# Kernel tuning notes

Measured on AMD Instinct MI355X. Metric: run time of the kernel, lower is better.

The kernel has to match this reference:

```python
import jax, jax.numpy as jnp
import numpy as np
import math

D = 768      # embedding_dim
H = 12       # attn_n_heads
HD = D // H  # head_dim = 64
F = 3072     # ff_latent_dim
B, S = 1, 4096
EPS = 1e-5


def setup_inputs() -> dict:
    key = jax.random.key(0)
    ks = jax.random.split(key, 16)
    s = 0.02
    return {
        "x": jax.random.normal(ks[0], (B, S, D), jnp.float32),
        # per-head Q/K/V projections stacked: [H, D, HD]
        "Wq": jax.random.normal(ks[1], (H, D, HD), jnp.float32) * s,
        "bq": jnp.zeros((H, HD), jnp.float32),
        "Wk": jax.random.normal(ks[2], (H, D, HD), jnp.float32) * s,
        "bk": jnp.zeros((H, HD), jnp.float32),
        "Wv": jax.random.normal(ks[3], (H, D, HD), jnp.float32) * s,
        "bv": jnp.zeros((H, HD), jnp.float32),
        "Wo": jax.random.normal(ks[4], (D, D), jnp.float32) * s,
        "bo": jnp.zeros((D,), jnp.float32),
        "ln1_w": jnp.ones((D,), jnp.float32),
        "ln1_b": jnp.zeros((D,), jnp.float32),
        "ln2_w": jnp.ones((D,), jnp.float32),
        "ln2_b": jnp.zeros((D,), jnp.float32),
        "W1": jax.random.normal(ks[5], (D, F), jnp.float32) * s,
        "b1": jnp.zeros((F,), jnp.float32),
        "W2": jax.random.normal(ks[6], (F, D), jnp.float32) * s,
        "b2": jnp.zeros((D,), jnp.float32),
    }


def _layer_norm(z, w, b):
    mu = jnp.mean(z, axis=-1, keepdims=True)
    var = jnp.mean(jnp.square(z - mu), axis=-1, keepdims=True)
    return (z - mu) * jax.lax.rsqrt(var + EPS) * w + b


def reference(x, Wq, bq, Wk, bk, Wv, bv, Wo, bo,
              ln1_w, ln1_b, ln2_w, ln2_b, W1, b1, W2, b2):
    # pre-norm attention block
    y = _layer_norm(x, ln1_w, ln1_b)
    q = jnp.einsum('bsd,hde->bhse', y, Wq) + bq[None, :, None, :]
    k = jnp.einsum('bsd,hde->bhse', y, Wk) + bk[None, :, None, :]
    v = jnp.einsum('bsd,hde->bhse', y, Wv) + bv[None, :, None, :]
    scores = jnp.einsum('bhqe,bhke->bhqk', q, k) * (1.0 / math.sqrt(HD))
    attn = jax.nn.softmax(scores, axis=-1)            # [B,H,S,S]
    o = jnp.einsum('bhqk,bhke->bhqe', attn, v)        # [B,H,S,HD]
    o = o.transpose(0, 2, 1, 3).reshape(x.shape[0], x.shape[1], D)  # concat heads
    o = o @ Wo + bo
    x = x + o
    # pre-norm FFN block (eval mode: dropout is identity)
    y = _layer_norm(x, ln2_w, ln2_b)
    h = jax.nn.gelu(y @ W1 + b1, approximate=False)   # torch F.gelu default = exact erf
    x = x + (h @ W2 + b2)
    return x
```

## Files before the change

### kernel.cpp

```cpp
#include <hip/hip_runtime.h>
#include <stdint.h>

typedef __bf16 bf16;
typedef __bf16 bf16x2 __attribute__((ext_vector_type(2)));
typedef __bf16 bf16x4 __attribute__((ext_vector_type(4)));
typedef __bf16 bf16x8 __attribute__((ext_vector_type(8)));
typedef float f32x4 __attribute__((ext_vector_type(4)));
typedef float f32x16 __attribute__((ext_vector_type(16)));
typedef uint32_t u32;
typedef unsigned int u32x2 __attribute__((ext_vector_type(2)));

#define QSCALE 0.1803368801111137f

__device__ __forceinline__ float fast_exp2(float x) {
#if __has_builtin(__builtin_amdgcn_exp2f)
  return __builtin_amdgcn_exp2f(x);
#else
  return exp2f(x);
#endif
}

__device__ __forceinline__ u32 pack_bf16(float a, float b) {
  bf16x2 v; v[0] = (bf16)a; v[1] = (bf16)b;
  return __builtin_bit_cast(u32, v);
}

__device__ __forceinline__ void permswap32(u32& a, u32& b) {
#if __has_builtin(__builtin_amdgcn_permlane32_swap)
  u32x2 r = __builtin_amdgcn_permlane32_swap(a, b, false, false);
  a = r[0]; b = r[1];
#else
  asm volatile("v_permlane32_swap_b32 %0, %1" : "+v"(a), "+v"(b));
#endif
}

__device__ __forceinline__ void async16(void* lds, const void* g) {
  __builtin_amdgcn_global_load_lds(
      (__attribute__((address_space(1))) uint32_t*)(uintptr_t)g,
      (__attribute__((address_space(3))) uint32_t*)(uint32_t)(uintptr_t)lds,
      16, 0, 0);
}

__global__ __launch_bounds__(256) void conv_qkv_w_kernel(
    const float* __restrict__ Wq, const float* __restrict__ Wk,
    const float* __restrict__ Wv, bf16* __restrict__ out)
{
  __shared__ float tile[32][33];
  int z = blockIdx.z;
  int part = z / 12, h = z - part * 12;
  const float* W = (part == 0) ? Wq : (part == 1) ? Wk : Wv;
  float sc = (part == 0) ? QSCALE : 1.0f;
  int bd = blockIdx.x * 32, be = blockIdx.y * 32;
  int tc = threadIdx.x & 31, tr = threadIdx.x >> 5;
  #pragma unroll
  for (int i = 0; i < 4; i++)
    tile[tr + i * 8][tc] = W[((size_t)h * 768 + bd + tr + i * 8) * 64 + be + tc] * sc;
  __syncthreads();
  #pragma unroll
  for (int i = 0; i < 4; i++) {
    int e = be + tr + i * 8;
    out[(size_t)(part * 768 + h * 64 + e) * 768 + bd + tc] = (bf16)tile[tc][tr + i * 8];
  }
}

__global__ __launch_bounds__(256) void conv_qkv_b_kernel(
    const float* __restrict__ bq, const float* __restrict__ bk,
    const float* __restrict__ bv, float* __restrict__ out)
{
  int n = blockIdx.x * 256 + threadIdx.x;
  int part = n / 768, nn = n - part * 768;
  const float* B = (part == 0) ? bq : (part == 1) ? bk : bv;
  float v = B[nn];
  if (part == 0) v *= QSCALE;
  out[n] = v;
}

__global__ __launch_bounds__(256) void transpose_tile_kernel(
    const float* __restrict__ in, bf16* __restrict__ out, int R, int C)
{
  __shared__ float tile[32][33];
  int bc = blockIdx.x * 32, br = blockIdx.y * 32;
  int tc = threadIdx.x & 31, tr = threadIdx.x >> 5;
  #pragma unroll
  for (int i = 0; i < 4; i++)
    tile[tr + i * 8][tc] = in[(size_t)(br + tr + i * 8) * C + bc + tc];
  __syncthreads();
  #pragma unroll
  for (int i = 0; i < 4; i++) {
    int c = bc + tr + i * 8;
    out[(size_t)c * R + br + tc] = (bf16)tile[tc][tr + i * 8];
  }
}

__global__ __launch_bounds__(256) void reduce_add_kernel(
    float* __restrict__ out, const bf16* __restrict__ p)
{
  int i = blockIdx.x * 256 + threadIdx.x;
  float4 o = ((float4*)out)[i];
  bf16x4 v = ((const bf16x4*)p)[i];
  o.x += (float)v[0]; o.y += (float)v[1];
  o.z += (float)v[2]; o.w += (float)v[3];
  ((float4*)out)[i] = o;
}

__global__ __launch_bounds__(256) void ln_kernel(
    const float* __restrict__ x, const float* __restrict__ w,
    const float* __restrict__ b, bf16* __restrict__ y)
{
  int row = blockIdx.x;
  const float* xr = x + (size_t)row * 768;
  int t = threadIdx.x;
  float v0 = xr[t], v1 = xr[t + 256], v2 = xr[t + 512];
  float s = v0 + v1 + v2, s2 = v0 * v0 + v1 * v1 + v2 * v2;
  #pragma unroll
  for (int d = 1; d < 64; d <<= 1) {
    s  += __shfl_xor(s, d, 64);
    s2 += __shfl_xor(s2, d, 64);
  }
  __shared__ float red[8];
  int wv = t >> 6, ln = t & 63;
  if (ln == 0) { red[wv] = s; red[4 + wv] = s2; }
  __syncthreads();
  s  = red[0] + red[1] + red[2] + red[3];
  s2 = red[4] + red[5] + red[6] + red[7];
  float mu = s * (1.0f / 768.0f);
  float var = s2 * (1.0f / 768.0f) - mu * mu;
  float rstd = rsqrtf(var + 1e-5f);
  bf16* yr = y + (size_t)row * 768;
  yr[t]       = (bf16)((v0 - mu) * rstd * w[t]       + b[t]);
  yr[t + 256] = (bf16)((v1 - mu) * rstd * w[t + 256] + b[t + 256]);
  yr[t + 512] = (bf16)((v2 - mu) * rstd * w[t + 512] + b[t + 512]);
}

__global__ __launch_bounds__(256) void ln_add_kernel(
    float* __restrict__ x1, const bf16* __restrict__ p,
    const float* __restrict__ w, const float* __restrict__ b,
    bf16* __restrict__ y)
{
  int row = blockIdx.x;
  float* xr = x1 + (size_t)row * 768;
  const bf16* pr = p + (size_t)row * 768;
  int t = threadIdx.x;
  float v0 = xr[t]       + (float)pr[t];
  float v1 = xr[t + 256] + (float)pr[t + 256];
  float v2 = xr[t + 512] + (float)pr[t + 512];
  xr[t] = v0; xr[t + 256] = v1; xr[t + 512] = v2;
  float s = v0 + v1 + v2, s2 = v0 * v0 + v1 * v1 + v2 * v2;
  #pragma unroll
  for (int d = 1; d < 64; d <<= 1) {
    s  += __shfl_xor(s, d, 64);
    s2 += __shfl_xor(s2, d, 64);
  }
  __shared__ float red[8];
  int wv = t >> 6, ln = t & 63;
  if (ln == 0) { red[wv] = s; red[4 + wv] = s2; }
  __syncthreads();
  s  = red[0] + red[1] + red[2] + red[3];
  s2 = red[4] + red[5] + red[6] + red[7];
  float mu = s * (1.0f / 768.0f);
  float var = s2 * (1.0f / 768.0f) - mu * mu;
  float rstd = rsqrtf(var + 1e-5f);
  bf16* yr = y + (size_t)row * 768;
  yr[t]       = (bf16)((v0 - mu) * rstd * w[t]       + b[t]);
  yr[t + 256] = (bf16)((v1 - mu) * rstd * w[t + 256] + b[t + 256]);
  yr[t + 512] = (bf16)((v2 - mu) * rstd * w[t + 512] + b[t + 512]);
}

template <int MODE>
__global__ __launch_bounds__(256) void gemm_bt(
    const bf16* __restrict__ A, const bf16* __restrict__ Bt,
    const float* __restrict__ bias, const float* __restrict__ res,
    void* __restrict__ outp, void* __restrict__ out2, int M, int N, int K)
{
  __shared__ bf16 As[128 * 32];
  __shared__ bf16 Bs[128 * 32];
  int t = threadIdx.x;
  int w = t >> 6, lane = t & 63;
  int quad = lane >> 4, l16 = lane & 15;
  int tile_m = blockIdx.y * 128, tile_n = blockIdx.x * 128;

  int srow = lane >> 2;
  int skb = (lane & 3) * 8;
  const bf16* Ag = A  + (size_t)(tile_m + w * 16 + srow) * K + skb;
  const bf16* Bg = Bt + (size_t)(tile_n + w * 16 + srow) * K + skb;
  char* AsB = (char*)As + w * 1024;
  char* BsB = (char*)Bs + w * 1024;
  size_t rstep = (size_t)64 * K;

  int wm = (w >> 1) * 64, wn = (w & 1) * 64;
  f32x4 acc[4][4] = {};

  int kbeg = 0, kend = K;
  if (MODE == 5) {
    int half = K >> 1;
    kbeg = blockIdx.z * half;
    kend = kbeg + half;
  }

  for (int k0 = kbeg; k0 < kend; k0 += 32) {
    __syncthreads();
    async16(AsB,        Ag + k0);
    async16(AsB + 4096, Ag + rstep + k0);
    async16(BsB,        Bg + k0);
    async16(BsB + 4096, Bg + rstep + k0);
    __syncthreads();

    bf16x8 af[4], bfr[4];
    #pragma unroll
    for (int mb = 0; mb < 4; mb++)
      af[mb] = *(const bf16x8*)(As + (wm + mb * 16 + l16) * 32 + quad * 8);
    #pragma unroll
    for (int nb = 0; nb < 4; nb++)
      bfr[nb] = *(const bf16x8*)(Bs + (wn + nb * 16 + l16) * 32 + quad * 8);
    #pragma unroll
    for (int mb = 0; mb < 4; mb++)
      #pragma unroll
      for (int nb = 0; nb < 4; nb++)
        acc[mb][nb] = __builtin_amdgcn_mfma_f32_16x16x32_bf16(
            af[mb], bfr[nb], acc[mb][nb], 0, 0, 0);
  }

  #pragma unroll
  for (int mb = 0; mb < 4; mb++) {
    #pragma unroll
    for (int nb = 0; nb < 4; nb++) {
      int col = tile_n + wn + nb * 16 + l16;
      int row0 = tile_m + wm + mb * 16 + quad * 4;
      if (MODE == 4) {
        float bc = bias[col];
        if (col < 1536) {
          #pragma unroll
          for (int r = 0; r < 4; r++)
            ((bf16*)outp)[(size_t)(row0 + r) * 1536 + col] =
                (bf16)(acc[mb][nb][r] + bc);
        } else {
          bf16x4 pk;
          #pragma unroll
          for (int r = 0; r < 4; r++) pk[r] = (bf16)(acc[mb][nb][r] + bc);
          *(bf16x4*)((bf16*)out2 + (size_t)(col - 1536) * 4096 + row0) = pk;
        }
      } else if (MODE == 2) {
        float bc = bias[col];
        #pragma unroll
        for (int r = 0; r < 4; r++) {
          size_t idx = (size_t)(row0 + r) * N + col;
          float v = acc[mb][nb][r] + bc;
          float g = 0.5f * v * (1.0f + erff(v * 0.70710678118654752f));
          ((bf16*)outp)[idx] = (bf16)g;
        }
      } else {
        if (blockIdx.z == 0) {
          float bc = bias[col];
          #pragma unroll
          for (int r = 0; r < 4; r++) {
            size_t idx = (size_t)(row0 + r) * N + col;
            ((float*)outp)[idx] = res[idx] + acc[mb][nb][r] + bc;
          }
        } else {
          #pragma unroll
          for (int r = 0; r < 4; r++) {
            size_t idx = (size_t)(row0 + r) * N + col;
            ((bf16*)out2)[idx] = (bf16)acc[mb][nb][r];
          }
        }
      }
    }
  }
}

__global__ __launch_bounds__(256) void flash_kernel(
    const bf16* __restrict__ qk, const bf16* __restrict__ vtg,
    bf16* __restrict__ Opart, float* __restrict__ Lpart)
{
  __shared__ char smem[49152];
  bf16* Qs = (bf16*)smem;
  int t = threadIdx.x, w = t >> 6, lane = t & 63;
  int l32 = lane & 31, hi = lane >> 5;
  int qt = blockIdx.x, h = blockIdx.y, z = blockIdx.z;
  int q0 = qt * 128, kv0 = z * 2048;
  int qsel = w & 1, ksel = w >> 1;
  int qw = qsel * 64, kb = ksel * 32;

  int srow = lane >> 3, scol = ((lane & 7) ^ srow) * 8;

  #pragma unroll
  for (int c = 0; c < 4; c++) {
    const bf16* qg = qk + (size_t)(q0 + c * 32 + w * 8 + srow) * 1536 + h * 64 + scol;
    async16(smem + c * 4096 + w * 1024, qg);
  }

  const bf16* kg = qk + 768 + h * 64 + (size_t)(kv0 + w * 8 + srow) * 1536 + scol;
  const bf16* vg = vtg + (size_t)(h * 64 + w * 8 + srow) * 4096 + kv0 + scol;

  {
    char* kb0 = smem + 16384 + w * 1024;
    char* vb0 = smem + 32768 + w * 1024;
    async16(kb0,        kg);
    async16(kb0 + 4096, kg + (size_t)32 * 1536);
    async16(vb0,        vg);
    async16(vb0 + 4096, vg + (size_t)32 * 4096);
  }
  __syncthreads();

  int qr0 = qw + l32, qr1 = qw + 32 + l32;
  bf16x8 qf0[4], qf1[4];
  #pragma unroll
  for (int ks = 0; ks < 4; ks++) {
    qf0[ks] = *(const bf16x8*)(Qs + qr0 * 64 + (((ks * 2 + hi) ^ (qr0 & 7)) * 8));
    qf1[ks] = *(const bf16x8*)(Qs + qr1 * 64 + (((ks * 2 + hi) ^ (qr1 & 7)) * 8));
  }

  f32x16 oT00 = {}, oT10 = {}, oT01 = {}, oT11 = {};
  float l0 = 0.0f, l1 = 0.0f;
  int krow = kb + l32;
  int er0 = l32, er1 = 32 + l32;

  for (int j = 0; j < 32; j++) {
    int cur = j & 1;
    if (j < 31) {
      const bf16* kgn = kg + (size_t)(j + 1) * 64 * 1536;
      const bf16* vgn = vg + (j + 1) * 64;
      char* kbn = smem + 16384 + (cur ^ 1) * 8192 + w * 1024;
      char* vbn = smem + 32768 + (cur ^ 1) * 8192 + w * 1024;
      async16(kbn,        kgn);
      async16(kbn + 4096, kgn + (size_t)32 * 1536);
      async16(vbn,        vgn);
      async16(vbn + 4096, vgn + (size_t)32 * 4096);
    }
    const bf16* Ks = (const bf16*)(smem + 16384 + cur * 8192);
    const bf16* Vs = (const bf16*)(smem + 32768 + cur * 8192);

    f32x16 s0 = {}, s1 = {};
    __builtin_amdgcn_s_setprio(1);
    #pragma unroll
    for (int ks = 0; ks < 4; ks++) {
      bf16x8 kf = *(const bf16x8*)(Ks + krow * 64 + (((ks * 2 + hi) ^ (krow & 7)) * 8));
      s0 = __builtin_amdgcn_mfma_f32_32x32x16_bf16(kf, qf0[ks], s0, 0, 0, 0);
      s1 = __builtin_amdgcn_mfma_f32_32x32x16_bf16(kf, qf1[ks], s1, 0, 0, 0);
    }
    __builtin_amdgcn_s_setprio(0);

    bf16x8 pf00, pf01, pf10, pf11;
    {
      float p[16];
      #pragma unroll
      for (int i = 0; i < 16; i++) p[i] = fast_exp2(s0[i]);
      float t0 = (p[0] + p[1]) + (p[2] + p[3]);
      float t1 = (p[4] + p[5]) + (p[6] + p[7]);
      float t2 = (p[8] + p[9]) + (p[10] + p[11]);
      float t3 = (p[12] + p[13]) + (p[14] + p[15]);
      l0 += (t0 + t1) + (t2 + t3);
      u32 dd[8];
      #pragma unroll
      for (int k = 0; k < 8; k++) dd[k] = pack_bf16(p[2 * k], p[2 * k + 1]);
      permswap32(dd[0], dd[2]);
      permswap32(dd[1], dd[3]);
      permswap32(dd[4], dd[6]);
      permswap32(dd[5], dd[7]);
      pf00 = __builtin_bit_cast(bf16x8, uint4{dd[0], dd[1], dd[2], dd[3]});
      pf01 = __builtin_bit_cast(bf16x8, uint4{dd[4], dd[5], dd[6], dd[7]});
    }
    {
      float p[16];
      #pragma unroll
      for (int i = 0; i < 16; i++) p[i] = fast_exp2(s1[i]);
      float t0 = (p[0] + p[1]) + (p[2] + p[3]);
      float t1 = (p[4] + p[5]) + (p[6] + p[7]);
      float t2 = (p[8] + p[9]) + (p[10] + p[11]);
      float t3 = (p[12] + p[13]) + (p[14] + p[15]);
      l1 += (t0 + t1) + (t2 + t3);
      u32 dd[8];
      #pragma unroll
      for (int k = 0; k < 8; k++) dd[k] = pack_bf16(p[2 * k], p[2 * k + 1]);
      permswap32(dd[0], dd[2]);
      permswap32(dd[1], dd[3]);
      permswap32(dd[4], dd[6]);
      permswap32(dd[5], dd[7]);
      pf10 = __builtin_bit_cast(bf16x8, uint4{dd[0], dd[1], dd[2], dd[3]});
      pf11 = __builtin_bit_cast(bf16x8, uint4{dd[4], dd[5], dd[6], dd[7]});
    }

    __builtin_amdgcn_s_setprio(1);
    #pragma unroll
    for (int kstep = 0; kstep < 2; kstep++) {
      int grp = (kb >> 3) + kstep * 2 + hi;
      bf16x8 va = *(const bf16x8*)(Vs + er0 * 64 + ((grp ^ (er0 & 7)) * 8));
      bf16x8 vb = *(const bf16x8*)(Vs + er1 * 64 + ((grp ^ (er1 & 7)) * 8));
      bf16x8 pa = kstep ? pf01 : pf00;
      bf16x8 pb = kstep ? pf11 : pf10;
      oT00 = __builtin_amdgcn_mfma_f32_32x32x16_bf16(va, pa, oT00, 0, 0, 0);
      oT10 = __builtin_amdgcn_mfma_f32_32x32x16_bf16(vb, pa, oT10, 0, 0, 0);
      oT01 = __builtin_amdgcn_mfma_f32_32x32x16_bf16(va, pb, oT01, 0, 0, 0);
      oT11 = __builtin_amdgcn_mfma_f32_32x32x16_bf16(vb, pb, oT11, 0, 0, 0);
    }
    __builtin_amdgcn_s_setprio(0);

    __syncthreads();
  }

  float lq0 = l0 + __shfl_xor(l0, 32, 64);
  float lq1 = l1 + __shfl_xor(l1, 32, 64);
  float* OS = (float*)smem;
  float* LS = (float*)(smem + 34304);
  if (ksel == 1) {
    #pragma unroll
    for (int i = 0; i < 16; i++) {
      int eoff = (i & 3) + 8 * (i >> 2) + 4 * hi;
      OS[qr0 * 67 + eoff]      = oT00[i];
      OS[qr0 * 67 + 32 + eoff] = oT10[i];
      OS[qr1 * 67 + eoff]      = oT01[i];
      OS[qr1 * 67 + 32 + eoff] = oT11[i];
    }
    if (hi == 0) { LS[qr0] = lq0; LS[qr1] = lq1; }
  }
  __syncthreads();
  if (ksel == 0) {
    size_t tb = ((size_t)z * 12 + h) * 32 + qt;
    float la0 = lq0 + LS[qr0], la1 = lq1 + LS[qr1];
    if (hi == 0) { Lpart[tb * 128 + qr0] = la0; Lpart[tb * 128 + qr1] = la1; }
    bf16* ob0 = Opart + tb * 8192 + (size_t)qr0 * 64;
    bf16* ob1 = Opart + tb * 8192 + (size_t)qr1 * 64;
    #pragma unroll
    for (int g = 0; g < 4; g++) {
      int e0 = 8 * g + 4 * hi;
      bf16x4 a0, a1, b0, b1;
      #pragma unroll
      for (int r = 0; r < 4; r++) {
        a0[r] = (bf16)(oT00[g * 4 + r] + OS[qr0 * 67 + e0 + r]);
        a1[r] = (bf16)(oT10[g * 4 + r] + OS[qr0 * 67 + 32 + e0 + r]);
        b0[r] = (bf16)(oT01[g * 4 + r] + OS[qr1 * 67 + e0 + r]);
        b1[r] = (bf16)(oT11[g * 4 + r] + OS[qr1 * 67 + 32 + e0 + r]);
      }
      *(bf16x4*)(ob0 + e0)      = a0;
      *(bf16x4*)(ob0 + 32 + e0) = a1;
      *(bf16x4*)(ob1 + e0)      = b0;
      *(bf16x4*)(ob1 + 32 + e0) = b1;
    }
  }
}

__global__ __launch_bounds__(256) void flash_combine_kernel(
    const bf16* __restrict__ Opart, const float* __restrict__ Lpart,
    bf16* __restrict__ o)
{
  int qt = blockIdx.x, h = blockIdx.y;
  int t = threadIdx.x;
  size_t t0 = (size_t)h * 32 + qt;
  size_t t1 = (size_t)(12 + h) * 32 + qt;
  #pragma unroll
  for (int qq = 0; qq < 2; qq++) {
    int q = qq * 64 + (t >> 2), eg = (t & 3) * 16;
    float inv = 1.0f / (Lpart[t0 * 128 + q] + Lpart[t1 * 128 + q]);
    const bf16* p0 = Opart + t0 * 8192 + (size_t)q * 64 + eg;
    const bf16* p1 = Opart + t1 * 8192 + (size_t)q * 64 + eg;
    bf16x8 a0 = *(const bf16x8*)p0, a1 = *(const bf16x8*)(p0 + 8);
    bf16x8 b0 = *(const bf16x8*)p1, b1 = *(const bf16x8*)(p1 + 8);
    bf16x8 r0, r1;
    #pragma unroll
    for (int i = 0; i < 8; i++) {
      r0[i] = (bf16)(((float)a0[i] + (float)b0[i]) * inv);
      r1[i] = (bf16)(((float)a1[i] + (float)b1[i]) * inv);
    }
    bf16* op = o + (size_t)(qt * 128 + q) * 768 + h * 64 + eg;
    *(bf16x8*)op       = r0;
    *(bf16x8*)(op + 8) = r1;
  }
}

extern "C" void kernel_launch(void* const* d_in, const int* in_sizes, int n_in,
                              void* d_out, int out_size, void* d_ws, size_t ws_size,
                              hipStream_t stream) {
  const float* x    = (const float*)d_in[0];
  const float* Wq   = (const float*)d_in[1];
  const float* bq   = (const float*)d_in[2];
  const float* Wk   = (const float*)d_in[3];
  const float* bk   = (const float*)d_in[4];
  const float* Wv   = (const float*)d_in[5];
  const float* bv   = (const float*)d_in[6];
  const float* Wo   = (const float*)d_in[7];
  const float* bo   = (const float*)d_in[8];
  const float* ln1w = (const float*)d_in[9];
  const float* ln1b = (const float*)d_in[10];
  const float* ln2w = (const float*)d_in[11];
  const float* ln2b = (const float*)d_in[12];
  const float* W1   = (const float*)d_in[13];
  const float* b1   = (const float*)d_in[14];
  const float* W2   = (const float*)d_in[15];
  const float* b2   = (const float*)d_in[16];
  float* out = (float*)d_out;

  char* ws = (char*)d_ws;
  bf16*  hbuf   = (bf16*)(ws + 0);
  float* Lpart  = (float*)(ws + 0);
  bf16*  ybuf   = (bf16*)(ws + 0);
  bf16*  qkbuf  = (bf16*)(ws + 6291456);
  bf16*  opar_o = (bf16*)(ws + 6291456);
  bf16*  vtg    = (bf16*)(ws + 18874368);
  float* x1     = (float*)(ws + 25165824);
  bf16*  Opart  = (bf16*)(ws + 25165824);
  bf16*  obuf   = (bf16*)(ws + 37748736);
  bf16*  y2buf  = obuf;
  bf16*  opar_f = obuf;
  bf16*  Wqkv_t = (bf16*)(ws + 44040192);
  bf16*  Wo_t   = (bf16*)(ws + 47579136);
  bf16*  W1_t   = (bf16*)(ws + 48758784);
  bf16*  W2_t   = (bf16*)(ws + 53477376);
  float* bqkv   = (float*)(ws + 58195968);

  conv_qkv_w_kernel<<<dim3(24, 2, 36), 256, 0, stream>>>(Wq, Wk, Wv, Wqkv_t);
  conv_qkv_b_kernel<<<9, 256, 0, stream>>>(bq, bk, bv, bqkv);
  transpose_tile_kernel<<<dim3(24, 24), 256, 0, stream>>>(Wo, Wo_t, 768, 768);
  transpose_tile_kernel<<<dim3(96, 24), 256, 0, stream>>>(W1, W1_t, 768, 3072);
  transpose_tile_kernel<<<dim3(24, 96), 256, 0, stream>>>(W2, W2_t, 3072, 768);

  ln_kernel<<<4096, 256, 0, stream>>>(x, ln1w, ln1b, ybuf);
  gemm_bt<4><<<dim3(18, 32), 256, 0, stream>>>(ybuf, Wqkv_t, bqkv,
                                               (const float*)nullptr, qkbuf, vtg,
                                               4096, 2304, 768);
  flash_kernel<<<dim3(32, 12, 2), 256, 0, stream>>>(qkbuf, vtg, Opart, Lpart);
  flash_combine_kernel<<<dim3(32, 12), 256, 0, stream>>>(Opart, Lpart, obuf);
  gemm_bt<5><<<dim3(6, 32, 2), 256, 0, stream>>>(obuf, Wo_t, bo, x, x1, opar_o,
                                                 4096, 768, 768);
  ln_add_kernel<<<4096, 256, 0, stream>>>(x1, opar_o, ln2w, ln2b, y2buf);
  gemm_bt<2><<<dim3(24, 32), 256, 0, stream>>>(y2buf, W1_t, b1,
                                               (const float*)nullptr, hbuf, nullptr,
                                               4096, 3072, 768);
  gemm_bt<5><<<dim3(6, 32, 2), 256, 0, stream>>>(hbuf, W2_t, b2, x1, out, opar_f,
                                                 4096, 768, 3072);
  reduce_add_kernel<<<3072, 256, 0, stream>>>(out, opar_f);
}
```

Before: 339.3 us.

## Merge prep kernels into one launch and double-buffer GEMM LDS tiles

Folds the weight transposes, QKV bias packing and the first layer norm into a single prep kernel dispatched by block index, which removes several launches and lets those small jobs run side by side. The GEMM now keeps two LDS buffers and issues the async loads for the next K slice before computing the current one, dropping one barrier per iteration. This doubles GEMM LDS use, and correctness depends on the global_load_lds writes having landed before the barrier that precedes their use.

```diff
diff --git a/kernel.cpp b/kernel.cpp
--- a/kernel.cpp
+++ b/kernel.cpp
@@ -41,46 +41,12 @@
       16, 0, 0);
 }
 
-__global__ __launch_bounds__(256) void conv_qkv_w_kernel(
-    const float* __restrict__ Wq, const float* __restrict__ Wk,
-    const float* __restrict__ Wv, bf16* __restrict__ out)
-{
-  __shared__ float tile[32][33];
-  int z = blockIdx.z;
-  int part = z / 12, h = z - part * 12;
-  const float* W = (part == 0) ? Wq : (part == 1) ? Wk : Wv;
-  float sc = (part == 0) ? QSCALE : 1.0f;
-  int bd = blockIdx.x * 32, be = blockIdx.y * 32;
-  int tc = threadIdx.x & 31, tr = threadIdx.x >> 5;
-  #pragma unroll
-  for (int i = 0; i < 4; i++)
-    tile[tr + i * 8][tc] = W[((size_t)h * 768 + bd + tr + i * 8) * 64 + be + tc] * sc;
-  __syncthreads();
-  #pragma unroll
-  for (int i = 0; i < 4; i++) {
-    int e = be + tr + i * 8;
-    out[(size_t)(part * 768 + h * 64 + e) * 768 + bd + tc] = (bf16)tile[tc][tr + i * 8];
-  }
-}
-
-__global__ __launch_bounds__(256) void conv_qkv_b_kernel(
-    const float* __restrict__ bq, const float* __restrict__ bk,
-    const float* __restrict__ bv, float* __restrict__ out)
-{
-  int n = blockIdx.x * 256 + threadIdx.x;
-  int part = n / 768, nn = n - part * 768;
-  const float* B = (part == 0) ? bq : (part == 1) ? bk : bv;
-  float v = B[nn];
-  if (part == 0) v *= QSCALE;
-  out[n] = v;
-}
-
-__global__ __launch_bounds__(256) void transpose_tile_kernel(
-    const float* __restrict__ in, bf16* __restrict__ out, int R, int C)
-{
-  __shared__ float tile[32][33];
-  int bc = blockIdx.x * 32, br = blockIdx.y * 32;
-  int tc = threadIdx.x & 31, tr = threadIdx.x >> 5;
+__device__ __forceinline__ void transpose_body(
+    const float* __restrict__ in, bf16* __restrict__ outp, int R, int C,
+    int bx, int by, float (*tile)[33], int t)
+{
+  int bc = bx * 32, br = by * 32;
+  int tc = t & 31, tr = t >> 5;
   #pragma unroll
   for (int i = 0; i < 4; i++)
     tile[tr + i * 8][tc] = in[(size_t)(br + tr + i * 8) * C + bc + tc];
@@ -88,7 +54,83 @@
   #pragma unroll
   for (int i = 0; i < 4; i++) {
     int c = bc + tr + i * 8;
-    out[(size_t)c * R + br + tc] = (bf16)tile[tc][tr + i * 8];
+    outp[(size_t)c * R + br + tc] = (bf16)tile[tc][tr + i * 8];
+  }
+}
+
+__global__ __launch_bounds__(256) void prep_kernel(
+    const float* __restrict__ x,
+    const float* __restrict__ ln1w, const float* __restrict__ ln1b,
+    const float* __restrict__ Wq, const float* __restrict__ Wk,
+    const float* __restrict__ Wv,
+    const float* __restrict__ Wo, const float* __restrict__ W1,
+    const float* __restrict__ W2,
+    const float* __restrict__ bq, const float* __restrict__ bk,
+    const float* __restrict__ bv,
+    bf16* __restrict__ ybuf, bf16* __restrict__ Wqkv_t,
+    bf16* __restrict__ Wo_t, bf16* __restrict__ W1_t, bf16* __restrict__ W2_t,
+    float* __restrict__ bqkv)
+{
+  __shared__ float tile[32][33];
+  int n = blockIdx.x;
+  int t = threadIdx.x;
+  if (n < 4096) {
+    int row = n;
+    const float* xr = x + (size_t)row * 768;
+    float v0 = xr[t], v1 = xr[t + 256], v2 = xr[t + 512];
+    float s = v0 + v1 + v2, s2 = v0 * v0 + v1 * v1 + v2 * v2;
+    #pragma unroll
+    for (int d = 1; d < 64; d <<= 1) {
+      s  += __shfl_xor(s, d, 64);
+      s2 += __shfl_xor(s2, d, 64);
+    }
+    float* red = &tile[0][0];
+    int wv = t >> 6, ln = t & 63;
+    if (ln == 0) { red[wv] = s; red[4 + wv] = s2; }
+    __syncthreads();
+    s  = red[0] + red[1] + red[2] + red[3];
+    s2 = red[4] + red[5] + red[6] + red[7];
+    float mu = s * (1.0f / 768.0f);
+    float var = s2 * (1.0f / 768.0f) - mu * mu;
+    float rstd = rsqrtf(var + 1e-5f);
+    bf16* yr = ybuf + (size_t)row * 768;
+    yr[t]       = (bf16)((v0 - mu) * rstd * ln1w[t]       + ln1b[t]);
+    yr[t + 256] = (bf16)((v1 - mu) * rstd * ln1w[t + 256] + ln1b[t + 256]);
+    yr[t + 512] = (bf16)((v2 - mu) * rstd * ln1w[t + 512] + ln1b[t + 512]);
+  } else if (n < 5824) {
+    int n2 = n - 4096;
+    int bz = n2 / 48, rem = n2 - bz * 48;
+    int by = rem / 24, bx = rem - by * 24;
+    int part = bz / 12, h = bz - part * 12;
+    const float* W = (part == 0) ? Wq : (part == 1) ? Wk : Wv;
+    float sc = (part == 0) ? QSCALE : 1.0f;
+    int bd = bx * 32, be = by * 32;
+    int tc = t & 31, tr = t >> 5;
+    #pragma unroll
+    for (int i = 0; i < 4; i++)
+      tile[tr + i * 8][tc] = W[((size_t)h * 768 + bd + tr + i * 8) * 64 + be + tc] * sc;
+    __syncthreads();
+    #pragma unroll
+    for (int i = 0; i < 4; i++) {
+      int e = be + tr + i * 8;
+      Wqkv_t[(size_t)(part * 768 + h * 64 + e) * 768 + bd + tc] = (bf16)tile[tc][tr + i * 8];
+    }
+  } else if (n < 6400) {
+    int m = n - 5824;
+    transpose_body(Wo, Wo_t, 768, 768, m % 24, m / 24, tile, t);
+  } else if (n < 8704) {
+    int m = n - 6400;
+    transpose_body(W1, W1_t, 768, 3072, m % 96, m / 96, tile, t);
+  } else if (n < 11008) {
+    int m = n - 8704;
+    transpose_body(W2, W2_t, 3072, 768, m % 24, m / 24, tile, t);
+  } else {
+    int idx = (n - 11008) * 256 + t;
+    int part = idx / 768, nn = idx - part * 768;
+    const float* B = (part == 0) ? bq : (part == 1) ? bk : bv;
+    float v = B[nn];
+    if (part == 0) v *= QSCALE;
+    bqkv[idx] = v;
   }
 }
 
@@ -103,14 +145,19 @@
   ((float4*)out)[i] = o;
 }
 
-__global__ __launch_bounds__(256) void ln_kernel(
-    const float* __restrict__ x, const float* __restrict__ w,
-    const float* __restrict__ b, bf16* __restrict__ y)
+__global__ __launch_bounds__(256) void ln_add_kernel(
+    float* __restrict__ x1, const bf16* __restrict__ p,
+    const float* __restrict__ w, const float* __restrict__ b,
+    bf16* __restrict__ y)
 {
   int row = blockIdx.x;
-  const float* xr = x + (size_t)row * 768;
+  float* xr = x1 + (size_t)row * 768;
+  const bf16* pr = p + (size_t)row * 768;
   int t = threadIdx.x;
-  float v0 = xr[t], v1 = xr[t + 256], v2 = xr[t + 512];
+  float v0 = xr[t]       + (float)pr[t];
+  float v1 = xr[t + 256] + (float)pr[t + 256];
+  float v2 = xr[t + 512] + (float)pr[t + 512];
+  xr[t] = v0; xr[t + 256] = v1; xr[t + 512] = v2;
   float s = v0 + v1 + v2, s2 = v0 * v0 + v1 * v1 + v2 * v2;
   #pragma unroll
   for (int d = 1; d < 64; d <<= 1) {
@@ -132,48 +179,14 @@
   yr[t + 512] = (bf16)((v2 - mu) * rstd * w[t + 512] + b[t + 512]);
 }
 
-__global__ __launch_bounds__(256) void ln_add_kernel(
-    float* __restrict__ x1, const bf16* __restrict__ p,
-    const float* __restrict__ w, const float* __restrict__ b,
-    bf16* __restrict__ y)
-{
-  int row = blockIdx.x;
-  float* xr = x1 + (size_t)row * 768;
-  const bf16* pr = p + (size_t)row * 768;
-  int t = threadIdx.x;
-  float v0 = xr[t]       + (float)pr[t];
-  float v1 = xr[t + 256] + (float)pr[t + 256];
-  float v2 = xr[t + 512] + (float)pr[t + 512];
-  xr[t] = v0; xr[t + 256] = v1; xr[t + 512] = v2;
-  float s = v0 + v1 + v2, s2 = v0 * v0 + v1 * v1 + v2 * v2;
-  #pragma unroll
-  for (int d = 1; d < 64; d <<= 1) {
-    s  += __shfl_xor(s, d, 64);
-    s2 += __shfl_xor(s2, d, 64);
-  }
-  __shared__ float red[8];
-  int wv = t >> 6, ln = t & 63;
-  if (ln == 0) { red[wv] = s; red[4 + wv] = s2; }
-  __syncthreads();
-  s  = red[0] + red[1] + red[2] + red[3];
-  s2 = red[4] + red[5] + red[6] + red[7];
-  float mu = s * (1.0f / 768.0f);
-  float var = s2 * (1.0f / 768.0f) - mu * mu;
-  float rstd = rsqrtf(var + 1e-5f);
-  bf16* yr = y + (size_t)row * 768;
-  yr[t]       = (bf16)((v0 - mu) * rstd * w[t]       + b[t]);
-  yr[t + 256] = (bf16)((v1 - mu) * rstd * w[t + 256] + b[t + 256]);
-  yr[t + 512] = (bf16)((v2 - mu) * rstd * w[t + 512] + b[t + 512]);
-}
-
 template <int MODE>
 __global__ __launch_bounds__(256) void gemm_bt(
     const bf16* __restrict__ A, const bf16* __restrict__ Bt,
     const float* __restrict__ bias, const float* __restrict__ res,
     void* __restrict__ outp, void* __restrict__ out2, int M, int N, int K)
 {
-  __shared__ bf16 As[128 * 32];
-  __shared__ bf16 Bs[128 * 32];
+  __shared__ bf16 As[2 * 128 * 32];
+  __shared__ bf16 Bs[2 * 128 * 32];
   int t = threadIdx.x;
   int w = t >> 6, lane = t & 63;
   int quad = lane >> 4, l16 = lane & 15;
@@ -197,27 +210,39 @@
     kend = kbeg + half;
   }
 
+  async16(AsB,        Ag + kbeg);
+  async16(AsB + 4096, Ag + rstep + kbeg);
+  async16(BsB,        Bg + kbeg);
+  async16(BsB + 4096, Bg + rstep + kbeg);
+
+  int cur = 0;
   for (int k0 = kbeg; k0 < kend; k0 += 32) {
     __syncthreads();
-    async16(AsB,        Ag + k0);
-    async16(AsB + 4096, Ag + rstep + k0);
-    async16(BsB,        Bg + k0);
-    async16(BsB + 4096, Bg + rstep + k0);
-    __syncthreads();
+    if (k0 + 32 < kend) {
+      char* An = AsB + (cur ^ 1) * 8192;
+      char* Bn = BsB + (cur ^ 1) * 8192;
+      async16(An,        Ag + k0 + 32);
+      async16(An + 4096, Ag + rstep + k0 + 32);
+      async16(Bn,        Bg + k0 + 32);
+      async16(Bn + 4096, Bg + rstep + k0 + 32);
+    }
+    const bf16* Ab = As + cur * 4096;
+    const bf16* Bb = Bs + cur * 4096;
 
     bf16x8 af[4], bfr[4];
     #pragma unroll
     for (int mb = 0; mb < 4; mb++)
-      af[mb] = *(const bf16x8*)(As + (wm + mb * 16 + l16) * 32 + quad * 8);
+      af[mb] = *(const bf16x8*)(Ab + (wm + mb * 16 + l16) * 32 + quad * 8);
     #pragma unroll
     for (int nb = 0; nb < 4; nb++)
-      bfr[nb] = *(const bf16x8*)(Bs + (wn + nb * 16 + l16) * 32 + quad * 8);
+      bfr[nb] = *(const bf16x8*)(Bb + (wn + nb * 16 + l16) * 32 + quad * 8);
     #pragma unroll
     for (int mb = 0; mb < 4; mb++)
       #pragma unroll
       for (int nb = 0; nb < 4; nb++)
         acc[mb][nb] = __builtin_amdgcn_mfma_f32_16x16x32_bf16(
             af[mb], bfr[nb], acc[mb][nb], 0, 0, 0);
+    cur ^= 1;
   }
 
   #pragma unroll
@@ -507,13 +532,9 @@
   bf16*  W2_t   = (bf16*)(ws + 53477376);
   float* bqkv   = (float*)(ws + 58195968);
 
-  conv_qkv_w_kernel<<<dim3(24, 2, 36), 256, 0, stream>>>(Wq, Wk, Wv, Wqkv_t);
-  conv_qkv_b_kernel<<<9, 256, 0, stream>>>(bq, bk, bv, bqkv);
-  transpose_tile_kernel<<<dim3(24, 24), 256, 0, stream>>>(Wo, Wo_t, 768, 768);
-  transpose_tile_kernel<<<dim3(96, 24), 256, 0, stream>>>(W1, W1_t, 768, 3072);
-  transpose_tile_kernel<<<dim3(24, 96), 256, 0, stream>>>(W2, W2_t, 3072, 768);
-
-  ln_kernel<<<4096, 256, 0, stream>>>(x, ln1w, ln1b, ybuf);
+  prep_kernel<<<11017, 256, 0, stream>>>(x, ln1w, ln1b, Wq, Wk, Wv, Wo, W1, W2,
+                                         bq, bk, bv,
+                                         ybuf, Wqkv_t, Wo_t, W1_t, W2_t, bqkv);
   gemm_bt<4><<<dim3(18, 32), 256, 0, stream>>>(ybuf, Wqkv_t, bqkv,
                                                (const float*)nullptr, qkbuf, vtg,
                                                4096, 2304, 768);
```

After: 311.0 us. 8.3% less time.
